# Kernel tuning notes

Measured on AMD Instinct MI355X. Metric: run time of the kernel, lower is better.

Reference implementation:

```python
import jax, jax.numpy as jnp
import numpy as np
from jax import lax

B, T, PRED_LEN = 1024, 100, 30
E, H, IN = 512, 1024, 2


def _gru_cell(h, gx, Whh, bhh):
    # PyTorch GRU cell. gx = x @ Wih.T + bih precomputed, shape (B, 3H).
    gh = h @ Whh.T + bhh
    gx_r, gx_z, gx_n = jnp.split(gx, 3, axis=-1)
    gh_r, gh_z, gh_n = jnp.split(gh, 3, axis=-1)
    r = jax.nn.sigmoid(gx_r + gh_r)
    z = jax.nn.sigmoid(gx_z + gh_z)
    n = jnp.tanh(gx_n + r * gh_n)
    return (1.0 - z) * n + z * h


def _run_gru(x, h0, Wih, Whh, bih, bhh):
    # x: (B, T, F) -> outputs (B, T, H), final hidden (B, H)
    gx = jnp.einsum('btf,gf->btg', x, Wih) + bih  # batch all input projections
    def step(h, gxt):
        h_new = _gru_cell(h, gxt, Whh, bhh)
        return h_new, h_new
    h_last, ys = lax.scan(step, h0, jnp.swapaxes(gx, 0, 1))
    return jnp.swapaxes(ys, 0, 1), h_last


def setup_inputs() -> dict:
    key = jax.random.key(0)
    ks = iter(jax.random.split(key, 32))
    s = 1.0 / np.sqrt(H)
    u = lambda k, shp: jax.random.uniform(k, shp, jnp.float32, -s, s)
    inp = {'obs': jax.random.normal(next(ks), (B, T, IN), jnp.float32)}
    inp['We'] = u(next(ks), (E, IN)); inp['be'] = u(next(ks), (E,))
    inp['Wed'] = u(next(ks), (E, 2)); inp['bed'] = u(next(ks), (E,))
    for name, fin in [('enc1', E), ('enc2', H), ('dec1', E), ('dec2', H)]:
        inp[name + '_Wih'] = u(next(ks), (3 * H, fin))
        inp[name + '_Whh'] = u(next(ks), (3 * H, H))
        inp[name + '_bih'] = u(next(ks), (3 * H,))
        inp[name + '_bhh'] = u(next(ks), (3 * H,))
    inp['Wout'] = u(next(ks), (2, H)); inp['bout'] = u(next(ks), (2,))
    return inp


def reference(obs, We, be, Wed, bed,
              enc1_Wih, enc1_Whh, enc1_bih, enc1_bhh,
              enc2_Wih, enc2_Whh, enc2_bih, enc2_bhh,
              dec1_Wih, dec1_Whh, dec1_bih, dec1_bhh,
              dec2_Wih, dec2_Whh, dec2_bih, dec2_bhh,
              Wout, bout):
    b = obs.shape[0]
    h0 = jnp.zeros((b, H), obs.dtype)
    # --- encoder ---
    emb = jnp.tanh(jnp.einsum('bti,ei->bte', obs, We) + be)
    enc1, h = _run_gru(emb, h0, enc1_Wih, enc1_Whh, enc1_bih, enc1_bhh)
    # quirk preserved: hidden from gru1 is fed as h0 of gru2
    enc2, h = _run_gru(enc1, h, enc2_Wih, enc2_Whh, enc2_bih, enc2_bhh)
    out_loc0 = enc2[:, -2, :] @ Wout.T + bout  # second-to-last step (B, 2)
    def dec_step(carry, _):
        hc, last = carry
        d_emb = jnp.tanh(last @ Wed.T + bed)
        h1 = _gru_cell(hc, d_emb @ dec1_Wih.T + dec1_bih, dec1_Whh, dec1_bhh)
        h2 = _gru_cell(h1, h1 @ dec2_Wih.T + dec2_bih, dec2_Whh, dec2_bhh)
        out = h2 @ Wout.T + bout
        return (h2, out), out
    _, preds = lax.scan(dec_step, (h, out_loc0), None, length=PRED_LEN)
    return jnp.swapaxes(preds, 0, 1)  # (B, pred_len, 2)
```

## Files before the change

kernel.cpp:

```cpp
#include <hip/hip_runtime.h>
#include <stdint.h>

#define NB 1024
#define NT 100
#define NPRED 30
#define NE 512
#define NH 1024
#define NG (3*NH)

typedef unsigned short u16;
typedef unsigned int u32;
typedef u16 u16x4 __attribute__((ext_vector_type(4)));
typedef float f32x4 __attribute__((ext_vector_type(4)));
typedef __bf16 bf16x8 __attribute__((ext_vector_type(8)));

__device__ __forceinline__ u16 f2b(float f){
  u32 u = __float_as_uint(f);
  u = (u + 0x7FFFu + ((u >> 16) & 1u)) >> 16;
  return (u16)u;
}
__device__ __forceinline__ float sig_(float x){ return 1.0f/(1.0f+__expf(-x)); }
__device__ __forceinline__ float tanh_(float x){
  float e = __expf(2.0f*fabsf(x));
  return copysignf(1.0f - 2.0f/(e+1.0f), x);
}

__global__ void cvt_kernel(const float* src, u16* dst, int n4){
  int i = blockIdx.x*256 + threadIdx.x;
  if (i < n4){
    f32x4 v = ((const f32x4*)src)[i];
    u16x4 o;
    o[0]=f2b(v[0]); o[1]=f2b(v[1]); o[2]=f2b(v[2]); o[3]=f2b(v[3]);
    ((u16x4*)dst)[i] = o;
  }
}

__global__ void emb_kernel(const float* __restrict__ obs, const float* __restrict__ Wei,
                           const float* __restrict__ bei, u16* __restrict__ out, int t){
  int idx = blockIdx.x*256 + threadIdx.x;
  int b = idx >> 9, e = idx & 511;
  float x0 = obs[(b*NT + t)*2], x1 = obs[(b*NT + t)*2 + 1];
  out[idx] = f2b(tanh_(Wei[e*2]*x0 + Wei[e*2+1]*x1 + bei[e]));
}

__global__ void demb_kernel(const float* __restrict__ last, const float* __restrict__ Wed,
                            const float* __restrict__ bed, u16* __restrict__ out){
  int idx = blockIdx.x*256 + threadIdx.x;
  int b = idx >> 9, e = idx & 511;
  out[idx] = f2b(tanh_(Wed[e*2]*last[b*2] + Wed[e*2+1]*last[b*2+1] + bed[e]));
}

__device__ __forceinline__ void gload16(const u16* g, const u16* lds){
  __builtin_amdgcn_global_load_lds(
      (const __attribute__((address_space(1))) void*)g,
      (__attribute__((address_space(3))) void*)lds, 16, 0, 0);
}

__global__ __launch_bounds__(256)
void gemm_dual_kernel(
  const u16* A0, int lda0, int K0, const u16* W0, const float* bias0, float* C0,
  const u16* A1, int lda1, int K1, const u16* W1, const float* bias1, float* C1)
{
  const u16* A; const u16* W; const float* bias; float* C; int lda, K;
  if (blockIdx.z == 0){ A=A0; lda=lda0; K=K0; W=W0; bias=bias0; C=C0; }
  else                { A=A1; lda=lda1; K=K1; W=W1; bias=bias1; C=C1; }

  __shared__ __align__(16) u16 As[128][32];
  __shared__ __align__(16) u16 Bs[128][32];

  const int bRow = blockIdx.y * 128;
  const int bCol = blockIdx.x * 128;
  const int tid = threadIdx.x;
  const int w = tid >> 6, l = tid & 63;
  const int wm = w >> 1, wn = w & 1;
  const int lrow = l >> 2, lcol = (l & 3) * 8;
  const int fr = l & 15, fk = (l >> 4) * 8;

  f32x4 acc[4][4];
  #pragma unroll
  for (int m=0;m<4;m++)
    #pragma unroll
    for (int n=0;n<4;n++) acc[m][n] = (f32x4)0.0f;

  const u16* Ab = A + (size_t)(bRow + lrow)*lda + lcol;
  const u16* Wb = W + (size_t)(bCol + lrow)*K   + lcol;

  for (int k0 = 0; k0 < K; k0 += 32){
    #pragma unroll
    for (int c=0;c<2;c++){
      int r0 = w*32 + c*16;
      gload16(Ab + (size_t)r0*lda + k0, &As[r0][0]);
      gload16(Wb + (size_t)r0*K   + k0, &Bs[r0][0]);
    }
    __syncthreads();

    bf16x8 af[4], bfr[4];
    #pragma unroll
    for (int m=0;m<4;m++) af[m]  = *(const bf16x8*)&As[wm*64 + m*16 + fr][fk];
    #pragma unroll
    for (int n=0;n<4;n++) bfr[n] = *(const bf16x8*)&Bs[wn*64 + n*16 + fr][fk];

    #pragma unroll
    for (int m=0;m<4;m++)
      #pragma unroll
      for (int n=0;n<4;n++)
        acc[m][n] = __builtin_amdgcn_mfma_f32_16x16x32_bf16(af[m], bfr[n], acc[m][n], 0, 0, 0);

    __syncthreads();
  }

  const int crow = (l >> 4) * 4, ccol = l & 15;
  #pragma unroll
  for (int n=0;n<4;n++){
    int col = bCol + wn*64 + n*16 + ccol;
    float bv = bias[col];
    #pragma unroll
    for (int m=0;m<4;m++){
      int row = bRow + wm*64 + m*16 + crow;
      float* Cp = C + (size_t)row*NG + col;
      #pragma unroll
      for (int r=0;r<4;r++) Cp[(size_t)r*NG] = acc[m][n][r] + bv;
    }
  }
}

__global__ void gru_cell_kernel(const float* __restrict__ gx, const float* __restrict__ gh,
                                const float* __restrict__ hin, float* __restrict__ hout,
                                u16* __restrict__ houtb, u16* __restrict__ seq)
{
  int idx = blockIdx.x*256 + threadIdx.x;
  int b = idx >> 8, jq = idx & 255;
  int base = b*768;
  const f32x4* gx4 = (const f32x4*)gx;
  const f32x4* gh4 = (const f32x4*)gh;
  f32x4 xr = gx4[base + jq], xz = gx4[base + 256 + jq], xn = gx4[base + 512 + jq];
  f32x4 hr = gh4[base + jq], hz = gh4[base + 256 + jq], hn = gh4[base + 512 + jq];
  f32x4 hv = ((const f32x4*)hin)[idx];
  f32x4 o; u16x4 ob;
  #pragma unroll
  for (int c=0;c<4;c++){
    float r = sig_(xr[c] + hr[c]);
    float z = sig_(xz[c] + hz[c]);
    float n = tanh_(xn[c] + r*hn[c]);
    float h = (1.0f - z)*n + z*hv[c];
    o[c] = h; ob[c] = f2b(h);
  }
  ((f32x4*)hout)[idx] = o;
  ((u16x4*)houtb)[idx] = ob;
  if (seq) ((u16x4*)seq)[idx] = ob;
}

__global__ void outproj_kernel(const float* __restrict__ h, const float* __restrict__ Wout,
                               const float* __restrict__ bout, float* __restrict__ last,
                               float* __restrict__ dout, int t)
{
  int b = blockIdx.x, tid = threadIdx.x;
  float s0 = 0.f, s1 = 0.f;
  const float* hb_ = h + (size_t)b*NH;
  for (int j = tid; j < NH; j += 256){
    float hv = hb_[j];
    s0 += hv * Wout[j];
    s1 += hv * Wout[NH + j];
  }
  #pragma unroll
  for (int off = 32; off > 0; off >>= 1){
    s0 += __shfl_down(s0, off);
    s1 += __shfl_down(s1, off);
  }
  __shared__ float red[8];
  int w = tid >> 6;
  if ((tid & 63) == 0){ red[w*2] = s0; red[w*2+1] = s1; }
  __syncthreads();
  if (tid == 0){
    float o0 = red[0]+red[2]+red[4]+red[6] + bout[0];
    float o1 = red[1]+red[3]+red[5]+red[7] + bout[1];
    last[b*2]   = o0;
    last[b*2+1] = o1;
    if (dout){ dout[(size_t)b*(NPRED*2) + t*2]     = o0;
               dout[(size_t)b*(NPRED*2) + t*2 + 1] = o1; }
  }
}

extern "C" void kernel_launch(void* const* d_in, const int* in_sizes, int n_in,
                              void* d_out, int out_size, void* d_ws, size_t ws_size,
                              hipStream_t stream)
{
  (void)in_sizes; (void)n_in; (void)out_size;
  const float* obs  = (const float*)d_in[0];
  const float* We   = (const float*)d_in[1];
  const float* be   = (const float*)d_in[2];
  const float* Wed  = (const float*)d_in[3];
  const float* bed  = (const float*)d_in[4];
  const float* e1Wih = (const float*)d_in[5];
  const float* e1Whh = (const float*)d_in[6];
  const float* e1bih = (const float*)d_in[7];
  const float* e1bhh = (const float*)d_in[8];
  const float* e2Wih = (const float*)d_in[9];
  const float* e2Whh = (const float*)d_in[10];
  const float* e2bih = (const float*)d_in[11];
  const float* e2bhh = (const float*)d_in[12];
  const float* d1Wih = (const float*)d_in[13];
  const float* d1Whh = (const float*)d_in[14];
  const float* d1bih = (const float*)d_in[15];
  const float* d1bhh = (const float*)d_in[16];
  const float* d2Wih = (const float*)d_in[17];
  const float* d2Whh = (const float*)d_in[18];
  const float* d2bih = (const float*)d_in[19];
  const float* d2bhh = (const float*)d_in[20];
  const float* Wout = (const float*)d_in[21];
  const float* bout = (const float*)d_in[22];
  float* out = (float*)d_out;

  char* ws = (char*)d_ws;
  size_t off = 0;
  auto alloc = [&](size_t bytes)->char* {
    char* p = ws + off;
    off += (bytes + 255) & ~(size_t)255;
    return p;
  };
  u16* wE1i = (u16*)alloc((size_t)NG*NE*2);
  u16* wE1h = (u16*)alloc((size_t)NG*NH*2);
  u16* wE2i = (u16*)alloc((size_t)NG*NH*2);
  u16* wE2h = (u16*)alloc((size_t)NG*NH*2);
  u16* wD1i = (u16*)alloc((size_t)NG*NE*2);
  u16* wD1h = (u16*)alloc((size_t)NG*NH*2);
  u16* wD2i = (u16*)alloc((size_t)NG*NH*2);
  u16* wD2h = (u16*)alloc((size_t)NG*NH*2);
  u16* embb  = (u16*)alloc((size_t)NB*NE*2);
  float* h1f = (float*)alloc((size_t)NB*NH*4);
  u16*   h1b = (u16*)alloc((size_t)NB*NH*2);
  float* h2f = (float*)alloc((size_t)NB*NH*4);
  u16*   h2b = (u16*)alloc((size_t)NB*NH*2);
  float* gx  = (float*)alloc((size_t)NB*NG*4);
  float* gh  = (float*)alloc((size_t)NB*NG*4);
  float* last = (float*)alloc((size_t)NB*2*4);

  const size_t slot_bytes = (size_t)NB*NH*2;
  size_t avail = (ws_size > off + (1u<<20)) ? (ws_size - off - (1u<<20)) : 0;
  int cache_steps = (int)(avail / slot_bytes);
  if (cache_steps > NT) cache_steps = NT;
  u16* cache = (u16*)alloc((size_t)cache_steps * slot_bytes);
  const int cache_start = NT - cache_steps;

  hipMemsetAsync(h1f, 0, (size_t)NB*NH*4, stream);
  hipMemsetAsync(h1b, 0, (size_t)NB*NH*2, stream);

  auto cvt = [&](const float* src, u16* dst, size_t n){
    int n4 = (int)(n >> 2);
    cvt_kernel<<<dim3((n4 + 255)/256), dim3(256), 0, stream>>>(src, dst, n4);
  };
  cvt(e1Wih, wE1i, (size_t)NG*NE);
  cvt(e1Whh, wE1h, (size_t)NG*NH);
  cvt(e2Wih, wE2i, (size_t)NG*NH);
  cvt(e2Whh, wE2h, (size_t)NG*NH);
  cvt(d1Wih, wD1i, (size_t)NG*NE);
  cvt(d1Whh, wD1h, (size_t)NG*NH);
  cvt(d2Wih, wD2i, (size_t)NG*NH);
  cvt(d2Whh, wD2h, (size_t)NG*NH);

  const dim3 gemm_grid(NG/128, NB/128, 2);
  const dim3 blk(256);
  const dim3 emb_grid((NB*NE)/256);
  const dim3 cell_grid((NB*NH/4)/256);

  for (int t = 0; t < NT; ++t){
    emb_kernel<<<emb_grid, blk, 0, stream>>>(obs, We, be, embb, t);
    gemm_dual_kernel<<<gemm_grid, blk, 0, stream>>>(
        embb, NE, NE, wE1i, e1bih, gx,
        h1b,  NH, NH, wE1h, e1bhh, gh);
    u16* slot = (t >= cache_start) ? cache + (size_t)(t - cache_start)*NB*NH : (u16*)nullptr;
    gru_cell_kernel<<<cell_grid, blk, 0, stream>>>(gx, gh, h1f, h1f, h1b, slot);
  }

  hipMemcpyAsync(h2f, h1f, (size_t)NB*NH*4, hipMemcpyDeviceToDevice, stream);
  hipMemcpyAsync(h2b, h1b, (size_t)NB*NH*2, hipMemcpyDeviceToDevice, stream);

  hipMemsetAsync(h1f, 0, (size_t)NB*NH*4, stream);
  hipMemsetAsync(h1b, 0, (size_t)NB*NH*2, stream);
  for (int t = 0; t < NT; ++t){
    const u16* enc1_t;
    if (t < cache_start){
      emb_kernel<<<emb_grid, blk, 0, stream>>>(obs, We, be, embb, t);
      gemm_dual_kernel<<<gemm_grid, blk, 0, stream>>>(
          embb, NE, NE, wE1i, e1bih, gx,
          h1b,  NH, NH, wE1h, e1bhh, gh);
      gru_cell_kernel<<<cell_grid, blk, 0, stream>>>(gx, gh, h1f, h1f, h1b, (u16*)nullptr);
      enc1_t = h1b;
    } else {
      enc1_t = cache + (size_t)(t - cache_start)*NB*NH;
    }
    gemm_dual_kernel<<<gemm_grid, blk, 0, stream>>>(
        enc1_t, NH, NH, wE2i, e2bih, gx,
        h2b,    NH, NH, wE2h, e2bhh, gh);
    gru_cell_kernel<<<cell_grid, blk, 0, stream>>>(gx, gh, h2f, h2f, h2b, (u16*)nullptr);
    if (t == NT - 2){
      outproj_kernel<<<dim3(NB), blk, 0, stream>>>(h2f, Wout, bout, last, (float*)nullptr, 0);
    }
  }

  for (int t = 0; t < NPRED; ++t){
    demb_kernel<<<emb_grid, blk, 0, stream>>>(last, Wed, bed, embb);
    gemm_dual_kernel<<<gemm_grid, blk, 0, stream>>>(
        embb, NE, NE, wD1i, d1bih, gx,
        h2b,  NH, NH, wD1h, d1bhh, gh);
    gru_cell_kernel<<<cell_grid, blk, 0, stream>>>(gx, gh, h2f, h1f, h1b, (u16*)nullptr);
    gemm_dual_kernel<<<gemm_grid, blk, 0, stream>>>(
        h1b, NH, NH, wD2i, d2bih, gx,
        h1b, NH, NH, wD2h, d2bhh, gh);
    gru_cell_kernel<<<cell_grid, blk, 0, stream>>>(gx, gh, h1f, h2f, h2b, (u16*)nullptr);
    outproj_kernel<<<dim3(NB), blk, 0, stream>>>(h2f, Wout, bout, last, out, t);
  }
}
```

Baseline: 10.18 ms.

## Batch input projections over time chunks and split-K the recurrent GEMM

The input-to-hidden GEMMs of both encoder layers are now computed for a chunk of up to 25 timesteps at once in a single large GEMM, using buffered embeddings and gx buffers in the workspace. The per-step recurrent GEMM is split along K into two halves writing separate partial buffers, which the GRU cell kernel sums. This takes the input-projection half of each per-step dual GEMM off the serial critical path and amortises weight loads across timesteps. The cost is more workspace use, an extra partial-sum read in the cell kernel, and a cache/chunk sizing scheme that depends on the available workspace.

```diff
diff --git a/kernel.cpp b/kernel.cpp
--- a/kernel.cpp
+++ b/kernel.cpp
@@ -35,12 +35,21 @@
   }
 }
 
-__global__ void emb_kernel(const float* __restrict__ obs, const float* __restrict__ Wei,
-                           const float* __restrict__ bei, u16* __restrict__ out, int t){
+__global__ void embN_kernel(const float* __restrict__ obs, const float* __restrict__ We,
+                            const float* __restrict__ be, u16* __restrict__ out, int t0){
+  int idx = blockIdx.x*256 + threadIdx.x;
+  int e = idx & 511, rb = idx >> 9;
+  int tc = rb >> 10, b = rb & 1023;
+  float x0 = obs[(b*NT + t0 + tc)*2], x1 = obs[(b*NT + t0 + tc)*2 + 1];
+  out[idx] = f2b(tanh_(We[e*2]*x0 + We[e*2+1]*x1 + be[e]));
+}
+
+__global__ void emb_kernel(const float* __restrict__ obs, const float* __restrict__ We,
+                           const float* __restrict__ be, u16* __restrict__ out, int t){
   int idx = blockIdx.x*256 + threadIdx.x;
   int b = idx >> 9, e = idx & 511;
   float x0 = obs[(b*NT + t)*2], x1 = obs[(b*NT + t)*2 + 1];
-  out[idx] = f2b(tanh_(Wei[e*2]*x0 + Wei[e*2+1]*x1 + bei[e]));
+  out[idx] = f2b(tanh_(We[e*2]*x0 + We[e*2+1]*x1 + be[e]));
 }
 
 __global__ void demb_kernel(const float* __restrict__ last, const float* __restrict__ Wed,
@@ -56,20 +65,15 @@
       (__attribute__((address_space(3))) void*)lds, 16, 0, 0);
 }
 
-__global__ __launch_bounds__(256)
-void gemm_dual_kernel(
-  const u16* A0, int lda0, int K0, const u16* W0, const float* bias0, float* C0,
-  const u16* A1, int lda1, int K1, const u16* W1, const float* bias1, float* C1)
-{
-  const u16* A; const u16* W; const float* bias; float* C; int lda, K;
-  if (blockIdx.z == 0){ A=A0; lda=lda0; K=K0; W=W0; bias=bias0; C=C0; }
-  else                { A=A1; lda=lda1; K=K1; W=W1; bias=bias1; C=C1; }
-
+__device__ __forceinline__ void gemm_tile_body(
+    const u16* __restrict__ A, int lda,
+    const u16* __restrict__ W, int ldw, int K,
+    const float* __restrict__ bias, float* __restrict__ C,
+    int bRow, int bCol)
+{
   __shared__ __align__(16) u16 As[128][32];
   __shared__ __align__(16) u16 Bs[128][32];
 
-  const int bRow = blockIdx.y * 128;
-  const int bCol = blockIdx.x * 128;
   const int tid = threadIdx.x;
   const int w = tid >> 6, l = tid & 63;
   const int wm = w >> 1, wn = w & 1;
@@ -83,14 +87,14 @@
     for (int n=0;n<4;n++) acc[m][n] = (f32x4)0.0f;
 
   const u16* Ab = A + (size_t)(bRow + lrow)*lda + lcol;
-  const u16* Wb = W + (size_t)(bCol + lrow)*K   + lcol;
+  const u16* Wb = W + (size_t)(bCol + lrow)*ldw + lcol;
 
   for (int k0 = 0; k0 < K; k0 += 32){
     #pragma unroll
     for (int c=0;c<2;c++){
       int r0 = w*32 + c*16;
       gload16(Ab + (size_t)r0*lda + k0, &As[r0][0]);
-      gload16(Wb + (size_t)r0*K   + k0, &Bs[r0][0]);
+      gload16(Wb + (size_t)r0*ldw + k0, &Bs[r0][0]);
     }
     __syncthreads();
 
@@ -113,7 +117,7 @@
   #pragma unroll
   for (int n=0;n<4;n++){
     int col = bCol + wn*64 + n*16 + ccol;
-    float bv = bias[col];
+    float bv = bias ? bias[col] : 0.0f;
     #pragma unroll
     for (int m=0;m<4;m++){
       int row = bRow + wm*64 + m*16 + crow;
@@ -124,7 +128,37 @@
   }
 }
 
-__global__ void gru_cell_kernel(const float* __restrict__ gx, const float* __restrict__ gh,
+__global__ __launch_bounds__(256)
+void gemm_big_kernel(const u16* A, int lda, int K, const u16* W,
+                     const float* bias, float* C)
+{
+  gemm_tile_body(A, lda, W, K, K, bias, C, blockIdx.y*128, blockIdx.x*128);
+}
+
+__global__ __launch_bounds__(256)
+void gemm_splitk_kernel(const u16* A, const u16* W, const float* bias,
+                        float* C0, float* C1)
+{
+  int z = blockIdx.z;
+  gemm_tile_body(A + z*512, NH, W + z*512, NH, 512,
+                 z ? nullptr : bias, z ? C1 : C0,
+                 blockIdx.y*128, blockIdx.x*128);
+}
+
+__global__ __launch_bounds__(256)
+void gemm_dual_kernel(
+  const u16* A0, int lda0, int K0, const u16* W0, const float* bias0, float* C0,
+  const u16* A1, int lda1, int K1, const u16* W1, const float* bias1, float* C1)
+{
+  if (blockIdx.z == 0)
+    gemm_tile_body(A0, lda0, W0, K0, K0, bias0, C0, blockIdx.y*128, blockIdx.x*128);
+  else
+    gemm_tile_body(A1, lda1, W1, K1, K1, bias1, C1, blockIdx.y*128, blockIdx.x*128);
+}
+
+__global__ void gru_cell_kernel(const float* __restrict__ gx,
+                                const float* __restrict__ gh0,
+                                const float* __restrict__ gh1,
                                 const float* __restrict__ hin, float* __restrict__ hout,
                                 u16* __restrict__ houtb, u16* __restrict__ seq)
 {
@@ -132,9 +166,13 @@
   int b = idx >> 8, jq = idx & 255;
   int base = b*768;
   const f32x4* gx4 = (const f32x4*)gx;
-  const f32x4* gh4 = (const f32x4*)gh;
+  const f32x4* g04 = (const f32x4*)gh0;
   f32x4 xr = gx4[base + jq], xz = gx4[base + 256 + jq], xn = gx4[base + 512 + jq];
-  f32x4 hr = gh4[base + jq], hz = gh4[base + 256 + jq], hn = gh4[base + 512 + jq];
+  f32x4 hr = g04[base + jq], hz = g04[base + 256 + jq], hn = g04[base + 512 + jq];
+  if (gh1){
+    const f32x4* g14 = (const f32x4*)gh1;
+    hr += g14[base + jq]; hz += g14[base + 256 + jq]; hn += g14[base + 512 + jq];
+  }
   f32x4 hv = ((const f32x4*)hin)[idx];
   f32x4 o; u16x4 ob;
   #pragma unroll
@@ -231,16 +269,25 @@
   u16*   h1b = (u16*)alloc((size_t)NB*NH*2);
   float* h2f = (float*)alloc((size_t)NB*NH*4);
   u16*   h2b = (u16*)alloc((size_t)NB*NH*2);
-  float* gx  = (float*)alloc((size_t)NB*NG*4);
-  float* gh  = (float*)alloc((size_t)NB*NG*4);
+  float* ghA = (float*)alloc((size_t)NB*NG*4);
+  float* ghB = (float*)alloc((size_t)NB*NG*4);
   float* last = (float*)alloc((size_t)NB*2*4);
 
-  const size_t slot_bytes = (size_t)NB*NH*2;
-  size_t avail = (ws_size > off + (1u<<20)) ? (ws_size - off - (1u<<20)) : 0;
-  int cache_steps = (int)(avail / slot_bytes);
-  if (cache_steps > NT) cache_steps = NT;
-  u16* cache = (u16*)alloc((size_t)cache_steps * slot_bytes);
-  const int cache_start = NT - cache_steps;
+  const size_t slot = (size_t)NB*NH*2;
+  const size_t chunk_unit = (size_t)NB*NE*2 + (size_t)NB*NG*4 + 512;
+  size_t rem = (ws_size > off) ? ws_size - off : 0;
+  int cs = 0, C = 1;
+  if (rem > chunk_unit + (1u<<20)){
+    size_t rem2 = rem - chunk_unit - (1u<<20);
+    cs = (int)(rem2 / slot); if (cs > NT) cs = NT;
+    rem2 -= (size_t)cs * slot;
+    C = 1 + (int)(rem2 / chunk_unit);
+    if (C > 25) C = 25; if (C > NT) C = NT;
+  }
+  u16* cache = (u16*)alloc((size_t)cs * slot);
+  u16* embc  = (u16*)alloc((size_t)C*NB*NE*2);
+  float* gxbuf = (float*)alloc((size_t)C*NB*NG*4);
+  const int cache_start = NT - cs;
 
   hipMemsetAsync(h1f, 0, (size_t)NB*NH*4, stream);
   hipMemsetAsync(h1b, 0, (size_t)NB*NH*2, stream);
@@ -258,56 +305,69 @@
   cvt(d2Wih, wD2i, (size_t)NG*NH);
   cvt(d2Whh, wD2h, (size_t)NG*NH);
 
-  const dim3 gemm_grid(NG/128, NB/128, 2);
   const dim3 blk(256);
+  const dim3 splitk_grid(NG/128, NB/128, 2);
+  const dim3 dual_grid(NG/128, NB/128, 2);
   const dim3 emb_grid((NB*NE)/256);
   const dim3 cell_grid((NB*NH/4)/256);
 
-  for (int t = 0; t < NT; ++t){
-    emb_kernel<<<emb_grid, blk, 0, stream>>>(obs, We, be, embb, t);
-    gemm_dual_kernel<<<gemm_grid, blk, 0, stream>>>(
-        embb, NE, NE, wE1i, e1bih, gx,
-        h1b,  NH, NH, wE1h, e1bhh, gh);
-    u16* slot = (t >= cache_start) ? cache + (size_t)(t - cache_start)*NB*NH : (u16*)nullptr;
-    gru_cell_kernel<<<cell_grid, blk, 0, stream>>>(gx, gh, h1f, h1f, h1b, slot);
+  for (int t0 = 0; t0 < NT; t0 += C){
+    int Ce = (NT - t0 < C) ? NT - t0 : C;
+    embN_kernel<<<dim3(Ce*2048), blk, 0, stream>>>(obs, We, be, embc, t0);
+    gemm_big_kernel<<<dim3(NG/128, Ce*8), blk, 0, stream>>>(embc, NE, NE, wE1i, e1bih, gxbuf);
+    for (int tc = 0; tc < Ce; ++tc){
+      int t = t0 + tc;
+      gemm_splitk_kernel<<<splitk_grid, blk, 0, stream>>>(h1b, wE1h, e1bhh, ghA, ghB);
+      u16* slot_p = (t >= cache_start) ? cache + (size_t)(t - cache_start)*NB*NH : (u16*)nullptr;
+      gru_cell_kernel<<<cell_grid, blk, 0, stream>>>(
+          gxbuf + (size_t)tc*NB*NG, ghA, ghB, h1f, h1f, h1b, slot_p);
+    }
   }
 
   hipMemcpyAsync(h2f, h1f, (size_t)NB*NH*4, hipMemcpyDeviceToDevice, stream);
   hipMemcpyAsync(h2b, h1b, (size_t)NB*NH*2, hipMemcpyDeviceToDevice, stream);
 
-  hipMemsetAsync(h1f, 0, (size_t)NB*NH*4, stream);
-  hipMemsetAsync(h1b, 0, (size_t)NB*NH*2, stream);
-  for (int t = 0; t < NT; ++t){
-    const u16* enc1_t;
-    if (t < cache_start){
-      emb_kernel<<<emb_grid, blk, 0, stream>>>(obs, We, be, embb, t);
-      gemm_dual_kernel<<<gemm_grid, blk, 0, stream>>>(
-          embb, NE, NE, wE1i, e1bih, gx,
-          h1b,  NH, NH, wE1h, e1bhh, gh);
-      gru_cell_kernel<<<cell_grid, blk, 0, stream>>>(gx, gh, h1f, h1f, h1b, (u16*)nullptr);
-      enc1_t = h1b;
-    } else {
-      enc1_t = cache + (size_t)(t - cache_start)*NB*NH;
-    }
-    gemm_dual_kernel<<<gemm_grid, blk, 0, stream>>>(
-        enc1_t, NH, NH, wE2i, e2bih, gx,
-        h2b,    NH, NH, wE2h, e2bhh, gh);
-    gru_cell_kernel<<<cell_grid, blk, 0, stream>>>(gx, gh, h2f, h2f, h2b, (u16*)nullptr);
-    if (t == NT - 2){
+  if (cache_start > 0){
+    hipMemsetAsync(h1f, 0, (size_t)NB*NH*4, stream);
+    hipMemsetAsync(h1b, 0, (size_t)NB*NH*2, stream);
+  }
+  for (int t = 0; t < cache_start; ++t){
+    emb_kernel<<<emb_grid, blk, 0, stream>>>(obs, We, be, embb, t);
+    gemm_dual_kernel<<<dual_grid, blk, 0, stream>>>(
+        embb, NE, NE, wE1i, e1bih, gxbuf,
+        h1b,  NH, NH, wE1h, e1bhh, ghA);
+    gru_cell_kernel<<<cell_grid, blk, 0, stream>>>(gxbuf, ghA, (float*)nullptr, h1f, h1f, h1b, (u16*)nullptr);
+    gemm_dual_kernel<<<dual_grid, blk, 0, stream>>>(
+        h1b, NH, NH, wE2i, e2bih, gxbuf,
+        h2b, NH, NH, wE2h, e2bhh, ghA);
+    gru_cell_kernel<<<cell_grid, blk, 0, stream>>>(gxbuf, ghA, (float*)nullptr, h2f, h2f, h2b, (u16*)nullptr);
+    if (t == NT - 2)
       outproj_kernel<<<dim3(NB), blk, 0, stream>>>(h2f, Wout, bout, last, (float*)nullptr, 0);
+  }
+  for (int t0 = cache_start; t0 < NT; t0 += C){
+    int Ce = (NT - t0 < C) ? NT - t0 : C;
+    gemm_big_kernel<<<dim3(NG/128, Ce*8), blk, 0, stream>>>(
+        cache + (size_t)(t0 - cache_start)*NB*NH, NH, NH, wE2i, e2bih, gxbuf);
+    for (int tc = 0; tc < Ce; ++tc){
+      int t = t0 + tc;
+      gemm_splitk_kernel<<<splitk_grid, blk, 0, stream>>>(h2b, wE2h, e2bhh, ghA, ghB);
+      gru_cell_kernel<<<cell_grid, blk, 0, stream>>>(
+          gxbuf + (size_t)tc*NB*NG, ghA, ghB, h2f, h2f, h2b, (u16*)nullptr);
+      if (t == NT - 2)
+        outproj_kernel<<<dim3(NB), blk, 0, stream>>>(h2f, Wout, bout, last, (float*)nullptr, 0);
     }
   }
 
   for (int t = 0; t < NPRED; ++t){
     demb_kernel<<<emb_grid, blk, 0, stream>>>(last, Wed, bed, embb);
-    gemm_dual_kernel<<<gemm_grid, blk, 0, stream>>>(
-        embb, NE, NE, wD1i, d1bih, gx,
-        h2b,  NH, NH, wD1h, d1bhh, gh);
-    gru_cell_kernel<<<cell_grid, blk, 0, stream>>>(gx, gh, h2f, h1f, h1b, (u16*)nullptr);
-    gemm_dual_kernel<<<gemm_grid, blk, 0, stream>>>(
-        h1b, NH, NH, wD2i, d2bih, gx,
-        h1b, NH, NH, wD2h, d2bhh, gh);
-    gru_cell_kernel<<<cell_grid, blk, 0, stream>>>(gx, gh, h1f, h2f, h2b, (u16*)nullptr);
+    gemm_dual_kernel<<<dual_grid, blk, 0, stream>>>(
+        embb, NE, NE, wD1i, d1bih, gxbuf,
+        h2b,  NH, NH, wD1h, d1bhh, ghA);
+    gru_cell_kernel<<<cell_grid, blk, 0, stream>>>(gxbuf, ghA, (float*)nullptr, h2f, h1f, h1b, (u16*)nullptr);
+    gemm_dual_kernel<<<dual_grid, blk, 0, stream>>>(
+        h1b, NH, NH, wD2i, d2bih, gxbuf,
+        h1b, NH, NH, wD2h, d2bhh, ghA);
+    gru_cell_kernel<<<cell_grid, blk, 0, stream>>>(gxbuf, ghA, (float*)nullptr, h1f, h2f, h2b, (u16*)nullptr);
     outproj_kernel<<<dim3(NB), blk, 0, stream>>>(h2f, Wout, bout, last, out, t);
   }
 }
```

After: 12.12 ms. +19.1%, slower.

## Double-buffer GEMM tiles with BK=64 and XOR-swizzled LDS layout

Applied to the files above, without the earlier changes.

Rewrites the bf16 MFMA GEMM body to use a K-tile of 64 with two LDS buffers, so the global-to-LDS loads for the next tile are issued before the MFMAs on the current one. It also XOR-swizzles the LDS column chunks to cut bank conflicts on fragment reads, and halves the number of barrier pairs per K. LDS use grows to 64KB per block, which may reduce occupancy. The host loop is split into uncached and cached phases without changing semantics.

```diff
diff --git a/kernel.cpp b/kernel.cpp
--- a/kernel.cpp
+++ b/kernel.cpp
@@ -35,12 +35,12 @@
   }
 }
 
-__global__ void emb_kernel(const float* __restrict__ obs, const float* __restrict__ Wei,
-                           const float* __restrict__ bei, u16* __restrict__ out, int t){
+__global__ void emb_kernel(const float* __restrict__ obs, const float* __restrict__ We,
+                           const float* __restrict__ be, u16* __restrict__ out, int t){
   int idx = blockIdx.x*256 + threadIdx.x;
   int b = idx >> 9, e = idx & 511;
   float x0 = obs[(b*NT + t)*2], x1 = obs[(b*NT + t)*2 + 1];
-  out[idx] = f2b(tanh_(Wei[e*2]*x0 + Wei[e*2+1]*x1 + bei[e]));
+  out[idx] = f2b(tanh_(We[e*2]*x0 + We[e*2+1]*x1 + be[e]));
 }
 
 __global__ void demb_kernel(const float* __restrict__ last, const float* __restrict__ Wed,
@@ -56,25 +56,21 @@
       (__attribute__((address_space(3))) void*)lds, 16, 0, 0);
 }
 
-__global__ __launch_bounds__(256)
-void gemm_dual_kernel(
-  const u16* A0, int lda0, int K0, const u16* W0, const float* bias0, float* C0,
-  const u16* A1, int lda1, int K1, const u16* W1, const float* bias1, float* C1)
-{
-  const u16* A; const u16* W; const float* bias; float* C; int lda, K;
-  if (blockIdx.z == 0){ A=A0; lda=lda0; K=K0; W=W0; bias=bias0; C=C0; }
-  else                { A=A1; lda=lda1; K=K1; W=W1; bias=bias1; C=C1; }
-
-  __shared__ __align__(16) u16 As[128][32];
-  __shared__ __align__(16) u16 Bs[128][32];
-
-  const int bRow = blockIdx.y * 128;
-  const int bCol = blockIdx.x * 128;
+__device__ __forceinline__ void gemm_tile_body(
+    const u16* __restrict__ A, int lda,
+    const u16* __restrict__ W, int K,
+    const float* __restrict__ bias, float* __restrict__ C,
+    int bRow, int bCol)
+{
+  __shared__ __align__(16) u16 As[2][128][64];
+  __shared__ __align__(16) u16 Bs[2][128][64];
+
   const int tid = threadIdx.x;
   const int w = tid >> 6, l = tid & 63;
   const int wm = w >> 1, wn = w & 1;
-  const int lrow = l >> 2, lcol = (l & 3) * 8;
-  const int fr = l & 15, fk = (l >> 4) * 8;
+  const int fr = l & 15, lhi = l >> 4;
+  const int srow = l >> 3;
+  const int gcol = (((l & 7) ^ srow) * 8);
 
   f32x4 acc[4][4];
   #pragma unroll
@@ -82,34 +78,53 @@
     #pragma unroll
     for (int n=0;n<4;n++) acc[m][n] = (f32x4)0.0f;
 
-  const u16* Ab = A + (size_t)(bRow + lrow)*lda + lcol;
-  const u16* Wb = W + (size_t)(bCol + lrow)*K   + lcol;
-
-  for (int k0 = 0; k0 < K; k0 += 32){
+  const u16* Ab = A + (size_t)bRow*lda + gcol;
+  const u16* Wb = W + (size_t)bCol*K + gcol;
+  const int NK = K >> 6;
+
+  #pragma unroll
+  for (int s4=0;s4<4;s4++){
+    int slab = w*4 + s4;
+    int row = slab*8 + srow;
+    gload16(Ab + (size_t)row*lda, &As[0][slab*8][0]);
+    gload16(Wb + (size_t)row*K,   &Bs[0][slab*8][0]);
+  }
+  __syncthreads();
+
+  for (int t = 0; t < NK; ++t){
+    const int cur = t & 1;
+    if (t + 1 < NK){
+      const int k0 = (t+1)*64;
+      #pragma unroll
+      for (int s4=0;s4<4;s4++){
+        int slab = w*4 + s4;
+        int row = slab*8 + srow;
+        gload16(Ab + (size_t)row*lda + k0, &As[cur^1][slab*8][0]);
+        gload16(Wb + (size_t)row*K   + k0, &Bs[cur^1][slab*8][0]);
+      }
+    }
+    const u16* Ac = &As[cur][0][0];
+    const u16* Bc = &Bs[cur][0][0];
     #pragma unroll
-    for (int c=0;c<2;c++){
-      int r0 = w*32 + c*16;
-      gload16(Ab + (size_t)r0*lda + k0, &As[r0][0]);
-      gload16(Wb + (size_t)r0*K   + k0, &Bs[r0][0]);
+    for (int kk=0; kk<2; ++kk){
+      const int ch = (((kk*4 + lhi) ^ (l & 7)) * 8);
+      bf16x8 af[4], bfr[4];
+      #pragma unroll
+      for (int m=0;m<4;m++)
+        af[m] = *(const bf16x8*)(Ac + (size_t)(wm*64 + m*16 + fr)*64 + ch);
+      #pragma unroll
+      for (int n=0;n<4;n++)
+        bfr[n] = *(const bf16x8*)(Bc + (size_t)(wn*64 + n*16 + fr)*64 + ch);
+      #pragma unroll
+      for (int m=0;m<4;m++)
+        #pragma unroll
+        for (int n=0;n<4;n++)
+          acc[m][n] = __builtin_amdgcn_mfma_f32_16x16x32_bf16(af[m], bfr[n], acc[m][n], 0, 0, 0);
     }
     __syncthreads();
-
-    bf16x8 af[4], bfr[4];
-    #pragma unroll
-    for (int m=0;m<4;m++) af[m]  = *(const bf16x8*)&As[wm*64 + m*16 + fr][fk];
-    #pragma unroll
-    for (int n=0;n<4;n++) bfr[n] = *(const bf16x8*)&Bs[wn*64 + n*16 + fr][fk];
-
-    #pragma unroll
-    for (int m=0;m<4;m++)
-      #pragma unroll
-      for (int n=0;n<4;n++)
-        acc[m][n] = __builtin_amdgcn_mfma_f32_16x16x32_bf16(af[m], bfr[n], acc[m][n], 0, 0, 0);
-
-    __syncthreads();
-  }
-
-  const int crow = (l >> 4) * 4, ccol = l & 15;
+  }
+
+  const int crow = lhi * 4, ccol = l & 15;
   #pragma unroll
   for (int n=0;n<4;n++){
     int col = bCol + wn*64 + n*16 + ccol;
@@ -122,6 +137,17 @@
       for (int r=0;r<4;r++) Cp[(size_t)r*NG] = acc[m][n][r] + bv;
     }
   }
+}
+
+__global__ __launch_bounds__(256)
+void gemm_dual_kernel(
+  const u16* A0, int lda0, int K0, const u16* W0, const float* bias0, float* C0,
+  const u16* A1, int lda1, int K1, const u16* W1, const float* bias1, float* C1)
+{
+  if (blockIdx.z == 0)
+    gemm_tile_body(A0, lda0, W0, K0, bias0, C0, blockIdx.y*128, blockIdx.x*128);
+  else
+    gemm_tile_body(A1, lda1, W1, K1, bias1, C1, blockIdx.y*128, blockIdx.x*128);
 }
 
 __global__ void gru_cell_kernel(const float* __restrict__ gx, const float* __restrict__ gh,
@@ -235,12 +261,12 @@
   float* gh  = (float*)alloc((size_t)NB*NG*4);
   float* last = (float*)alloc((size_t)NB*2*4);
 
-  const size_t slot_bytes = (size_t)NB*NH*2;
+  const size_t slot = (size_t)NB*NH*2;
   size_t avail = (ws_size > off + (1u<<20)) ? (ws_size - off - (1u<<20)) : 0;
-  int cache_steps = (int)(avail / slot_bytes);
-  if (cache_steps > NT) cache_steps = NT;
-  u16* cache = (u16*)alloc((size_t)cache_steps * slot_bytes);
-  const int cache_start = NT - cache_steps;
+  int cs = (int)(avail / slot);
+  if (cs > NT) cs = NT;
+  u16* cache = (u16*)alloc((size_t)cs * slot);
+  const int cache_start = NT - cs;
 
   hipMemsetAsync(h1f, 0, (size_t)NB*NH*4, stream);
   hipMemsetAsync(h1b, 0, (size_t)NB*NH*2, stream);
@@ -258,53 +284,57 @@
   cvt(d2Wih, wD2i, (size_t)NG*NH);
   cvt(d2Whh, wD2h, (size_t)NG*NH);
 
-  const dim3 gemm_grid(NG/128, NB/128, 2);
   const dim3 blk(256);
+  const dim3 dual_grid(NG/128, NB/128, 2);
   const dim3 emb_grid((NB*NE)/256);
   const dim3 cell_grid((NB*NH/4)/256);
 
   for (int t = 0; t < NT; ++t){
     emb_kernel<<<emb_grid, blk, 0, stream>>>(obs, We, be, embb, t);
-    gemm_dual_kernel<<<gemm_grid, blk, 0, stream>>>(
+    gemm_dual_kernel<<<dual_grid, blk, 0, stream>>>(
         embb, NE, NE, wE1i, e1bih, gx,
         h1b,  NH, NH, wE1h, e1bhh, gh);
-    u16* slot = (t >= cache_start) ? cache + (size_t)(t - cache_start)*NB*NH : (u16*)nullptr;
-    gru_cell_kernel<<<cell_grid, blk, 0, stream>>>(gx, gh, h1f, h1f, h1b, slot);
+    u16* slot_p = (t >= cache_start) ? cache + (size_t)(t - cache_start)*NB*NH : (u16*)nullptr;
+    gru_cell_kernel<<<cell_grid, blk, 0, stream>>>(gx, gh, h1f, h1f, h1b, slot_p);
   }
 
   hipMemcpyAsync(h2f, h1f, (size_t)NB*NH*4, hipMemcpyDeviceToDevice, stream);
   hipMemcpyAsync(h2b, h1b, (size_t)NB*NH*2, hipMemcpyDeviceToDevice, stream);
 
-  hipMemsetAsync(h1f, 0, (size_t)NB*NH*4, stream);
-  hipMemsetAsync(h1b, 0, (size_t)NB*NH*2, stream);
-  for (int t = 0; t < NT; ++t){
-    const u16* enc1_t;
-    if (t < cache_start){
-      emb_kernel<<<emb_grid, blk, 0, stream>>>(obs, We, be, embb, t);
-      gemm_dual_kernel<<<gemm_grid, blk, 0, stream>>>(
-          embb, NE, NE, wE1i, e1bih, gx,
-          h1b,  NH, NH, wE1h, e1bhh, gh);
-      gru_cell_kernel<<<cell_grid, blk, 0, stream>>>(gx, gh, h1f, h1f, h1b, (u16*)nullptr);
-      enc1_t = h1b;
-    } else {
-      enc1_t = cache + (size_t)(t - cache_start)*NB*NH;
-    }
-    gemm_dual_kernel<<<gemm_grid, blk, 0, stream>>>(
+  if (cache_start > 0){
+    hipMemsetAsync(h1f, 0, (size_t)NB*NH*4, stream);
+    hipMemsetAsync(h1b, 0, (size_t)NB*NH*2, stream);
+  }
+  for (int t = 0; t < cache_start; ++t){
+    emb_kernel<<<emb_grid, blk, 0, stream>>>(obs, We, be, embb, t);
+    gemm_dual_kernel<<<dual_grid, blk, 0, stream>>>(
+        embb, NE, NE, wE1i, e1bih, gx,
+        h1b,  NH, NH, wE1h, e1bhh, gh);
+    gru_cell_kernel<<<cell_grid, blk, 0, stream>>>(gx, gh, h1f, h1f, h1b, (u16*)nullptr);
+    gemm_dual_kernel<<<dual_grid, blk, 0, stream>>>(
+        h1b, NH, NH, wE2i, e2bih, gx,
+        h2b, NH, NH, wE2h, e2bhh, gh);
+    gru_cell_kernel<<<cell_grid, blk, 0, stream>>>(gx, gh, h2f, h2f, h2b, (u16*)nullptr);
+    if (t == NT - 2)
+      outproj_kernel<<<dim3(NB), blk, 0, stream>>>(h2f, Wout, bout, last, (float*)nullptr, 0);
+  }
+  for (int t = cache_start; t < NT; ++t){
+    const u16* enc1_t = cache + (size_t)(t - cache_start)*NB*NH;
+    gemm_dual_kernel<<<dual_grid, blk, 0, stream>>>(
         enc1_t, NH, NH, wE2i, e2bih, gx,
         h2b,    NH, NH, wE2h, e2bhh, gh);
     gru_cell_kernel<<<cell_grid, blk, 0, stream>>>(gx, gh, h2f, h2f, h2b, (u16*)nullptr);
-    if (t == NT - 2){
+    if (t == NT - 2)
       outproj_kernel<<<dim3(NB), blk, 0, stream>>>(h2f, Wout, bout, last, (float*)nullptr, 0);
-    }
   }
 
   for (int t = 0; t < NPRED; ++t){
     demb_kernel<<<emb_grid, blk, 0, stream>>>(last, Wed, bed, embb);
-    gemm_dual_kernel<<<gemm_grid, blk, 0, stream>>>(
+    gemm_dual_kernel<<<dual_grid, blk, 0, stream>>>(
         embb, NE, NE, wD1i, d1bih, gx,
         h2b,  NH, NH, wD1h, d1bhh, gh);
     gru_cell_kernel<<<cell_grid, blk, 0, stream>>>(gx, gh, h2f, h1f, h1b, (u16*)nullptr);
-    gemm_dual_kernel<<<gemm_grid, blk, 0, stream>>>(
+    gemm_dual_kernel<<<dual_grid, blk, 0, stream>>>(
         h1b, NH, NH, wD2i, d2bih, gx,
         h1b, NH, NH, wD2h, d2bhh, gh);
     gru_cell_kernel<<<cell_grid, blk, 0, stream>>>(gx, gh, h1f, h2f, h2b, (u16*)nullptr);
```

Result: faster. 8.357 ms (-17.9%).
